# Kernel optimization log

Measured on AMD Instinct MI355X. Metric: run time of the kernel, lower is better.

## Reference

```python
import jax, jax.numpy as jnp
import numpy as np

N_POINTS, D_EMBED, N_CLUSTERS = 131072, 512, 512
ALPHA = 100.0   # softmax sharpness (python scalar in original forward)
LAMBD = 0.1     # loss weight (init arg in original)


def setup_inputs() -> dict:
    key = jax.random.key(0)
    k1, k2 = jax.random.split(key)
    embeddings = jax.random.normal(k1, (N_POINTS, D_EMBED), dtype=jnp.float32)
    centroids = jax.random.normal(k2, (N_CLUSTERS, D_EMBED), dtype=jnp.float32)
    alpha = jnp.float32(ALPHA)
    lambd = jnp.float32(LAMBD)
    return {"embeddings": embeddings, "centroids": centroids, "alpha": alpha, "lambd": lambd}


def reference(embeddings, centroids, alpha, lambd):
    # Squared euclidean distance to every centroid, computed via GEMM expansion
    # instead of the original per-centroid python loop:
    #   dist[n, k] = ||x_n||^2 - 2 x_n . c_k + ||c_k||^2
    x2 = jnp.sum(embeddings * embeddings, axis=1, keepdims=True)   # [N, 1]
    c2 = jnp.sum(centroids * centroids, axis=1)                    # [K]
    dist = x2 - 2.0 * (embeddings @ centroids.T) + c2[None, :]     # [N, K]
    # Original: exp(-alpha*(d - min_k d)) / sum == stable softmax of -alpha*d over k.
    w = jax.nn.softmax(-alpha * dist, axis=1)                      # [N, K]
    # lambd * mean over points of softmax-weighted distance sum over clusters.
    return lambd * jnp.mean(jnp.sum(dist * w, axis=1))
```

## Files before the change

kernel.cpp:

```cpp
#include <hip/hip_runtime.h>
#include <stdint.h>

#define NPTS   131072
#define DEMB   512
#define NCL    512
#define BM     64
#define NCHUNK 8
#define NTHREADS 256
#define NBLK   (NPTS / BM)

typedef __attribute__((ext_vector_type(4))) float f32x4;
typedef __attribute__((ext_vector_type(8))) short short8;
typedef __attribute__((ext_vector_type(8))) unsigned short us8;

#define WS_CB   0u
#define WS_C2   (512u * 1024u)
#define WS_PART (WS_C2 + 2048u)

static __device__ __forceinline__ unsigned short f2bf(float f) {
  union { float f; uint32_t u; } c{f};
  uint32_t r = c.u + 0x7FFFu + ((c.u >> 16) & 1u);
  return (unsigned short)(r >> 16);
}
static __device__ __forceinline__ float sq4(f32x4 v) {
  return v[0] * v[0] + v[1] * v[1] + v[2] * v[2] + v[3] * v[3];
}

#define LOAD_B8(DST, BASE)                                                     \
  do {                                                                         \
    const uint8_t* _b0 = (const uint8_t*)(BASE);                               \
    const uint8_t* _b1 = _b0 + 4096;                                           \
    asm volatile("global_load_dwordx4 %0, %8, off\n\t"                         \
                 "global_load_dwordx4 %1, %8, off offset:1024\n\t"             \
                 "global_load_dwordx4 %2, %8, off offset:2048\n\t"             \
                 "global_load_dwordx4 %3, %8, off offset:3072\n\t"             \
                 "global_load_dwordx4 %4, %9, off\n\t"                         \
                 "global_load_dwordx4 %5, %9, off offset:1024\n\t"             \
                 "global_load_dwordx4 %6, %9, off offset:2048\n\t"             \
                 "global_load_dwordx4 %7, %9, off offset:3072"                 \
                 : "=&v"(DST[0]), "=&v"(DST[1]), "=&v"(DST[2]), "=&v"(DST[3]), \
                   "=&v"(DST[4]), "=&v"(DST[5]), "=&v"(DST[6]), "=&v"(DST[7])  \
                 : "v"(_b0), "v"(_b1)                                          \
                 : "memory");                                                  \
  } while (0)

#define LOAD_E4(D, P)                                                          \
  asm volatile("global_load_dwordx4 %0, %4, off\n\t"                           \
               "global_load_dwordx4 %1, %4, off offset:16\n\t"                 \
               "global_load_dwordx4 %2, %4, off offset:32\n\t"                 \
               "global_load_dwordx4 %3, %4, off offset:48"                     \
               : "=&v"(D[0]), "=&v"(D[1]), "=&v"(D[2]), "=&v"(D[3])            \
               : "v"(P)                                                        \
               : "memory")

#define WAITV(N)                                                               \
  do {                                                                         \
    asm volatile("s_waitcnt vmcnt(" #N ")" ::: "memory");                      \
    __builtin_amdgcn_sched_barrier(0);                                         \
  } while (0)

#define BAR()                                                                  \
  do {                                                                         \
    asm volatile("s_waitcnt lgkmcnt(0)" ::: "memory");                         \
    __builtin_amdgcn_s_barrier();                                              \
  } while (0)

__global__ __launch_bounds__(128) void prep_kernel(const float* __restrict__ cent,
                                                   uint8_t* __restrict__ ws) {
  const int k = blockIdx.x;
  const int t = threadIdx.x;
  float4 v = ((const float4*)(cent + (size_t)k * DEMB))[t];
  float sq = v.x * v.x + v.y * v.y + v.z * v.z + v.w * v.w;
#pragma unroll
  for (int m = 1; m < 64; m <<= 1) sq += __shfl_xor(sq, m, 64);
  __shared__ float red[2];
  if ((t & 63) == 0) red[t >> 6] = sq;
  __syncthreads();
  if (t == 0) ((float*)(ws + WS_C2))[k] = red[0] + red[1];

  ushort4 b;
  b.x = f2bf(v.x); b.y = f2bf(v.y); b.z = f2bf(v.z); b.w = f2bf(v.w);
  const int d = t * 4;
  const int ch = d >> 6;
  const int dd = d & 63;
  const int kk = dd >> 5;
  const int lhi = (dd >> 3) & 3;
  const int elem = dd & 7;
  const int w = k >> 7;
  const int n = (k >> 4) & 7;
  const int l15 = k & 15;
  const int lane = lhi * 16 + l15;
  const uint32_t off =
      (uint32_t)((((ch * 4 + w) * 2 + kk) * 8 + n) * 64 + lane) * 16u +
      (uint32_t)elem * 2u;
  *(ushort4*)(ws + WS_CB + off) = b;
}

__global__ __launch_bounds__(NTHREADS, 2) void main_kernel(
    const float* __restrict__ emb, const uint8_t* __restrict__ ws,
    const float* __restrict__ alphap) {
  __shared__ uint8_t Ab[2][8192];
  __shared__ float redmin[256];
  __shared__ float redse[256];
  __shared__ float redsge[256];
  __shared__ float gmin[64];
  __shared__ float x2s[64];

  const int t = threadIdx.x;
  const int w = t >> 6;
  const int l = t & 63;
  const int l15 = l & 15;
  const int lhi = l >> 4;
  const int bid = blockIdx.x;
  const size_t row0 = (size_t)bid * BM;

  float* partials = (float*)(ws + WS_PART);

  f32x4 acc[4][8];
#pragma unroll
  for (int m = 0; m < 4; ++m)
#pragma unroll
    for (int n = 0; n < 8; ++n) acc[m][n] = (f32x4){0.f, 0.f, 0.f, 0.f};

  const int r = t >> 2;
  const int q = t & 3;
  const float* xge = emb + (row0 + r) * DEMB + q * 16;
  uint32_t xoff[2];
#pragma unroll
  for (int j = 0; j < 2; ++j)
    xoff[j] = (uint32_t)r * 128u + (uint32_t)(((2 * q + j) ^ (r & 7)) << 4);

  float x2a = 0.f;

  const uint8_t* fbw = ws + WS_CB + (uint32_t)w * 16384u + (uint32_t)l * 16u;

  short8 bf[16];
  f32x4 ev0[4], ev1[4];

#define STAGE_FROM(EV, DSTBUF)                                                 \
  do {                                                                         \
    uint8_t* _an = (DSTBUF);                                                   \
    _Pragma("unroll")                                                          \
    for (int j = 0; j < 2; ++j) {                                              \
      f32x4 a = EV[2 * j], b = EV[2 * j + 1];                                  \
      x2a += sq4(a) + sq4(b);                                                  \
      us8 u;                                                                   \
      u[0] = f2bf(a[0]); u[1] = f2bf(a[1]); u[2] = f2bf(a[2]); u[3] = f2bf(a[3]); \
      u[4] = f2bf(b[0]); u[5] = f2bf(b[1]); u[6] = f2bf(b[2]); u[7] = f2bf(b[3]); \
      *(us8*)(_an + xoff[j]) = u;                                              \
    }                                                                          \
  } while (0)

  LOAD_E4(ev0, xge);
  LOAD_E4(ev1, xge + 64);
  LOAD_B8((&bf[0]), fbw);
  LOAD_B8((&bf[8]), fbw + 8192);
  WAITV(20);
  STAGE_FROM(ev0, &Ab[0][0]);
  BAR();

#define CHUNK_BODY(CH, EVN, EVS, VN)                                           \
  {                                                                            \
    if ((CH) + 2 < NCHUNK)                                                     \
      LOAD_E4(EVN, xge + ((CH) + 2) * 64);                                     \
    const uint8_t* xb = &Ab[(CH) & 1][0];                                      \
    WAITV(VN);                                                                 \
    __builtin_amdgcn_s_setprio(1);                                             \
    _Pragma("unroll")                                                          \
    for (int kk = 0; kk < 2; ++kk) {                                           \
      const uint32_t swz = (uint32_t)(((kk * 4 + lhi) ^ (l15 & 7)) << 4);      \
      short8 af[4];                                                            \
      _Pragma("unroll")                                                        \
      for (int m = 0; m < 4; ++m)                                              \
        af[m] = *(const short8*)(xb + (uint32_t)(m * 16 + l15) * 128u + swz);  \
      _Pragma("unroll")                                                        \
      for (int m = 0; m < 4; ++m)                                              \
        _Pragma("unroll")                                                      \
        for (int n = 0; n < 8; ++n)                                            \
          acc[m][n] = __builtin_amdgcn_mfma_f32_16x16x32_bf16(                 \
              af[m], bf[kk * 8 + n], acc[m][n], 0, 0, 0);                      \
    }                                                                          \
    __builtin_amdgcn_s_setprio(0);                                             \
    if ((CH) + 1 < NCHUNK) {                                                   \
      STAGE_FROM(EVS, &Ab[((CH) + 1) & 1][0]);                                 \
      const uint8_t* nb = fbw + (uint32_t)((CH) + 1) * 65536u;                 \
      LOAD_B8((&bf[0]), nb);                                                   \
      LOAD_B8((&bf[8]), nb + 8192);                                            \
    }                                                                          \
    BAR();                                                                     \
  }

  CHUNK_BODY(0, ev0, ev1, 4)
  CHUNK_BODY(1, ev1, ev0, 4)
  CHUNK_BODY(2, ev0, ev1, 4)
  CHUNK_BODY(3, ev1, ev0, 4)
  CHUNK_BODY(4, ev0, ev1, 4)
  CHUNK_BODY(5, ev1, ev0, 4)
  CHUNK_BODY(6, ev0, ev1, 0)
  CHUNK_BODY(7, ev1, ev0, 0)
#undef CHUNK_BODY
#undef STAGE_FROM

  const float alpha = alphap[0];
  float c2r[8];
  {
    const float* c2p = (const float*)(ws + WS_C2) + w * 128 + l15;
    asm volatile("global_load_dword %0, %8, off\n\t"
                 "global_load_dword %1, %8, off offset:64\n\t"
                 "global_load_dword %2, %8, off offset:128\n\t"
                 "global_load_dword %3, %8, off offset:192\n\t"
                 "global_load_dword %4, %8, off offset:256\n\t"
                 "global_load_dword %5, %8, off offset:320\n\t"
                 "global_load_dword %6, %8, off offset:384\n\t"
                 "global_load_dword %7, %8, off offset:448"
                 : "=&v"(c2r[0]), "=&v"(c2r[1]), "=&v"(c2r[2]), "=&v"(c2r[3]),
                   "=&v"(c2r[4]), "=&v"(c2r[5]), "=&v"(c2r[6]), "=&v"(c2r[7])
                 : "v"(c2p)
                 : "memory");
    asm volatile("s_waitcnt vmcnt(0)" ::: "memory");
    __builtin_amdgcn_sched_barrier(0);
  }

  x2a += __shfl_xor(x2a, 1, 64);
  x2a += __shfl_xor(x2a, 2, 64);
  if ((l & 3) == 0) x2s[r] = x2a;

  float rmin[4][4];
#pragma unroll
  for (int m = 0; m < 4; ++m)
#pragma unroll
    for (int i = 0; i < 4; ++i) {
      float mn = c2r[0] - 2.f * acc[m][0][i];
#pragma unroll
      for (int n = 1; n < 8; ++n) mn = fminf(mn, c2r[n] - 2.f * acc[m][n][i]);
      rmin[m][i] = mn;
    }
#pragma unroll
  for (int msk = 1; msk < 16; msk <<= 1)
#pragma unroll
    for (int m = 0; m < 4; ++m)
#pragma unroll
      for (int i = 0; i < 4; ++i)
        rmin[m][i] = fminf(rmin[m][i], __shfl_xor(rmin[m][i], msk, 64));
  if (l15 == 0) {
#pragma unroll
    for (int m = 0; m < 4; ++m)
#pragma unroll
      for (int i = 0; i < 4; ++i)
        redmin[w * 64 + m * 16 + lhi * 4 + i] = rmin[m][i];
  }
  __syncthreads();
  if (t < 64) {
    float mn = redmin[t];
#pragma unroll
    for (int w2 = 1; w2 < 4; ++w2) mn = fminf(mn, redmin[w2 * 64 + t]);
    gmin[t] = mn;
  }
  __syncthreads();
#pragma unroll
  for (int m = 0; m < 4; ++m) {
#pragma unroll
    for (int i = 0; i < 4; ++i) {
      const int row = m * 16 + lhi * 4 + i;
      const float M = gmin[row];
      float se = 0.f, sge = 0.f;
#pragma unroll
      for (int n = 0; n < 8; ++n) {
        const float g = c2r[n] - 2.f * acc[m][n][i];
        const float gm = g - M;
        const float e = __expf(-alpha * gm);
        se += e;
        sge += gm * e;
      }
#pragma unroll
      for (int msk = 1; msk < 16; msk <<= 1) {
        se += __shfl_xor(se, msk, 64);
        sge += __shfl_xor(sge, msk, 64);
      }
      if (l15 == 0) {
        redse[w * 64 + row] = se;
        redsge[w * 64 + row] = sge;
      }
    }
  }
  __syncthreads();
  if (t < 64) {
    float Se = 0.f, Sge = 0.f;
#pragma unroll
    for (int w2 = 0; w2 < 4; ++w2) {
      Se += redse[w2 * 64 + t];
      Sge += redsge[w2 * 64 + t];
    }
    float v = gmin[t] + Sge / Se + x2s[t];
#pragma unroll
    for (int msk = 1; msk < 64; msk <<= 1) v += __shfl_xor(v, msk, 64);
    if (t == 0) partials[bid] = v;
  }
}

__global__ __launch_bounds__(256) void final_kernel(const uint8_t* __restrict__ ws,
                                                    const float* __restrict__ lambdp,
                                                    float* __restrict__ out) {
  const float* partials = (const float*)(ws + WS_PART);
  const int t = threadIdx.x;
  float s = 0.f;
  for (int i = t; i < NBLK; i += 256) s += partials[i];
#pragma unroll
  for (int msk = 1; msk < 64; msk <<= 1) s += __shfl_xor(s, msk, 64);
  __shared__ float red[4];
  if ((t & 63) == 0) red[t >> 6] = s;
  __syncthreads();
  if (t == 0)
    out[0] = lambdp[0] * (red[0] + red[1] + red[2] + red[3]) * (1.0f / (float)NPTS);
}

extern "C" void kernel_launch(void* const* d_in, const int* in_sizes, int n_in,
                              void* d_out, int out_size, void* d_ws, size_t ws_size,
                              hipStream_t stream) {
  const float* emb = (const float*)d_in[0];
  const float* cent = (const float*)d_in[1];
  const float* alphap = (const float*)d_in[2];
  const float* lambdp = (const float*)d_in[3];
  float* out = (float*)d_out;
  uint8_t* ws = (uint8_t*)d_ws;

  prep_kernel<<<NCL, 128, 0, stream>>>(cent, ws);
  main_kernel<<<NBLK, NTHREADS, 0, stream>>>(emb, ws, alphap);
  final_kernel<<<1, 256, 0, stream>>>(ws, lambdp, out);
}
```

Before: 104.0 us.

## Switch GEMM from bf16 to fp8 MFMA with double-buffered centroid fragments

```diff
diff --git a/kernel.cpp b/kernel.cpp
--- a/kernel.cpp
+++ b/kernel.cpp
@@ -10,39 +10,29 @@
 #define NBLK   (NPTS / BM)
 
 typedef __attribute__((ext_vector_type(4))) float f32x4;
-typedef __attribute__((ext_vector_type(8))) short short8;
-typedef __attribute__((ext_vector_type(8))) unsigned short us8;
 
 #define WS_CB   0u
-#define WS_C2   (512u * 1024u)
-#define WS_PART (WS_C2 + 2048u)
-
-static __device__ __forceinline__ unsigned short f2bf(float f) {
-  union { float f; uint32_t u; } c{f};
-  uint32_t r = c.u + 0x7FFFu + ((c.u >> 16) & 1u);
-  return (unsigned short)(r >> 16);
-}
+#define WS_C2   262144u
+#define WS_PART 264192u
+
 static __device__ __forceinline__ float sq4(f32x4 v) {
   return v[0] * v[0] + v[1] * v[1] + v[2] * v[2] + v[3] * v[3];
 }
 
-#define LOAD_B8(DST, BASE)                                                     \
-  do {                                                                         \
-    const uint8_t* _b0 = (const uint8_t*)(BASE);                               \
-    const uint8_t* _b1 = _b0 + 4096;                                           \
-    asm volatile("global_load_dwordx4 %0, %8, off\n\t"                         \
-                 "global_load_dwordx4 %1, %8, off offset:1024\n\t"             \
-                 "global_load_dwordx4 %2, %8, off offset:2048\n\t"             \
-                 "global_load_dwordx4 %3, %8, off offset:3072\n\t"             \
-                 "global_load_dwordx4 %4, %9, off\n\t"                         \
-                 "global_load_dwordx4 %5, %9, off offset:1024\n\t"             \
-                 "global_load_dwordx4 %6, %9, off offset:2048\n\t"             \
-                 "global_load_dwordx4 %7, %9, off offset:3072"                 \
-                 : "=&v"(DST[0]), "=&v"(DST[1]), "=&v"(DST[2]), "=&v"(DST[3]), \
-                   "=&v"(DST[4]), "=&v"(DST[5]), "=&v"(DST[6]), "=&v"(DST[7])  \
-                 : "v"(_b0), "v"(_b1)                                          \
-                 : "memory");                                                  \
-  } while (0)
+#define LOAD_B8F(DST, BASE)                                                    \
+  asm volatile("global_load_dwordx2 %0, %8, off\n\t"                           \
+               "global_load_dwordx2 %1, %8, off offset:512\n\t"                \
+               "global_load_dwordx2 %2, %8, off offset:1024\n\t"               \
+               "global_load_dwordx2 %3, %8, off offset:1536\n\t"               \
+               "global_load_dwordx2 %4, %8, off offset:2048\n\t"               \
+               "global_load_dwordx2 %5, %8, off offset:2560\n\t"               \
+               "global_load_dwordx2 %6, %8, off offset:3072\n\t"               \
+               "global_load_dwordx2 %7, %8, off offset:3584"                   \
+               : "=&v"((DST)[0]), "=&v"((DST)[1]), "=&v"((DST)[2]),            \
+                 "=&v"((DST)[3]), "=&v"((DST)[4]), "=&v"((DST)[5]),            \
+                 "=&v"((DST)[6]), "=&v"((DST)[7])                              \
+               : "v"(BASE)                                                     \
+               : "memory")
 
 #define LOAD_E4(D, P)                                                          \
   asm volatile("global_load_dwordx4 %0, %4, off\n\t"                           \
@@ -78,28 +68,27 @@
   __syncthreads();
   if (t == 0) ((float*)(ws + WS_C2))[k] = red[0] + red[1];
 
-  ushort4 b;
-  b.x = f2bf(v.x); b.y = f2bf(v.y); b.z = f2bf(v.z); b.w = f2bf(v.w);
+  int p = __builtin_amdgcn_cvt_pk_fp8_f32(v.x, v.y, 0, false);
+  p = __builtin_amdgcn_cvt_pk_fp8_f32(v.z, v.w, p, true);
+
   const int d = t * 4;
   const int ch = d >> 6;
   const int dd = d & 63;
   const int kk = dd >> 5;
   const int lhi = (dd >> 3) & 3;
-  const int elem = dd & 7;
   const int w = k >> 7;
   const int n = (k >> 4) & 7;
   const int l15 = k & 15;
   const int lane = lhi * 16 + l15;
-  const uint32_t off =
-      (uint32_t)((((ch * 4 + w) * 2 + kk) * 8 + n) * 64 + lane) * 16u +
-      (uint32_t)elem * 2u;
-  *(ushort4*)(ws + WS_CB + off) = b;
+  const uint32_t off = (uint32_t)(ch * 32768 + w * 8192 + kk * 4096 + n * 512 +
+                                  lane * 8 + (dd & 7));
+  *(uint32_t*)(ws + WS_CB + off) = (uint32_t)p;
 }
 
 __global__ __launch_bounds__(NTHREADS, 2) void main_kernel(
     const float* __restrict__ emb, const uint8_t* __restrict__ ws,
     const float* __restrict__ alphap) {
-  __shared__ uint8_t Ab[2][8192];
+  __shared__ uint8_t Ab[2][4096];
   __shared__ float redmin[256];
   __shared__ float redse[256];
   __shared__ float redsge[256];
@@ -128,13 +117,13 @@
   uint32_t xoff[2];
 #pragma unroll
   for (int j = 0; j < 2; ++j)
-    xoff[j] = (uint32_t)r * 128u + (uint32_t)(((2 * q + j) ^ (r & 7)) << 4);
+    xoff[j] = (uint32_t)r * 64u + (uint32_t)(((2 * q + j) ^ (r & 7)) << 3);
 
   float x2a = 0.f;
 
-  const uint8_t* fbw = ws + WS_CB + (uint32_t)w * 16384u + (uint32_t)l * 16u;
-
-  short8 bf[16];
+  const uint8_t* fbw = ws + WS_CB + (uint32_t)w * 8192u + (uint32_t)l * 8u;
+
+  long bA[16], bB[16];
   f32x4 ev0[4], ev1[4];
 
 #define STAGE_FROM(EV, DSTBUF)                                                 \
@@ -144,60 +133,65 @@
     for (int j = 0; j < 2; ++j) {                                              \
       f32x4 a = EV[2 * j], b = EV[2 * j + 1];                                  \
       x2a += sq4(a) + sq4(b);                                                  \
-      us8 u;                                                                   \
-      u[0] = f2bf(a[0]); u[1] = f2bf(a[1]); u[2] = f2bf(a[2]); u[3] = f2bf(a[3]); \
-      u[4] = f2bf(b[0]); u[5] = f2bf(b[1]); u[6] = f2bf(b[2]); u[7] = f2bf(b[3]); \
-      *(us8*)(_an + xoff[j]) = u;                                              \
+      uint2 u;                                                                 \
+      int p0 = __builtin_amdgcn_cvt_pk_fp8_f32(a[0], a[1], 0, false);          \
+      p0 = __builtin_amdgcn_cvt_pk_fp8_f32(a[2], a[3], p0, true);              \
+      int p1 = __builtin_amdgcn_cvt_pk_fp8_f32(b[0], b[1], 0, false);          \
+      p1 = __builtin_amdgcn_cvt_pk_fp8_f32(b[2], b[3], p1, true);              \
+      u.x = (uint32_t)p0;                                                      \
+      u.y = (uint32_t)p1;                                                      \
+      *(uint2*)(_an + xoff[j]) = u;                                            \
     }                                                                          \
   } while (0)
 
   LOAD_E4(ev0, xge);
   LOAD_E4(ev1, xge + 64);
-  LOAD_B8((&bf[0]), fbw);
-  LOAD_B8((&bf[8]), fbw + 8192);
+  LOAD_B8F(&bA[0], fbw);
+  LOAD_B8F(&bA[8], fbw + 4096);
   WAITV(20);
   STAGE_FROM(ev0, &Ab[0][0]);
   BAR();
 
-#define CHUNK_BODY(CH, EVN, EVS, VN)                                           \
+#define CHUNK_BODY(CH, BCUR, BNEXT, EVN, EVS, VN)                              \
   {                                                                            \
     if ((CH) + 2 < NCHUNK)                                                     \
       LOAD_E4(EVN, xge + ((CH) + 2) * 64);                                     \
+    if ((CH) + 1 < NCHUNK) {                                                   \
+      const uint8_t* nb = fbw + (uint32_t)((CH) + 1) * 32768u;                 \
+      LOAD_B8F(&BNEXT[0], nb);                                                 \
+      LOAD_B8F(&BNEXT[8], nb + 4096);                                          \
+    }                                                                          \
     const uint8_t* xb = &Ab[(CH) & 1][0];                                      \
     WAITV(VN);                                                                 \
     __builtin_amdgcn_s_setprio(1);                                             \
     _Pragma("unroll")                                                          \
     for (int kk = 0; kk < 2; ++kk) {                                           \
-      const uint32_t swz = (uint32_t)(((kk * 4 + lhi) ^ (l15 & 7)) << 4);      \
-      short8 af[4];                                                            \
+      const uint32_t swz = (uint32_t)(((kk * 4 + lhi) ^ (l15 & 7)) << 3);      \
+      long af[4];                                                              \
       _Pragma("unroll")                                                        \
       for (int m = 0; m < 4; ++m)                                              \
-        af[m] = *(const short8*)(xb + (uint32_t)(m * 16 + l15) * 128u + swz);  \
+        af[m] = *(const long*)(xb + (uint32_t)(m * 16 + l15) * 64u + swz);     \
       _Pragma("unroll")                                                        \
       for (int m = 0; m < 4; ++m)                                              \
         _Pragma("unroll")                                                      \
         for (int n = 0; n < 8; ++n)                                            \
-          acc[m][n] = __builtin_amdgcn_mfma_f32_16x16x32_bf16(                 \
-              af[m], bf[kk * 8 + n], acc[m][n], 0, 0, 0);                      \
+          acc[m][n] = __builtin_amdgcn_mfma_f32_16x16x32_fp8_fp8(              \
+              af[m], BCUR[kk * 8 + n], acc[m][n], 0, 0, 0);                    \
     }                                                                          \
     __builtin_amdgcn_s_setprio(0);                                             \
-    if ((CH) + 1 < NCHUNK) {                                                   \
+    if ((CH) + 1 < NCHUNK)                                                     \
       STAGE_FROM(EVS, &Ab[((CH) + 1) & 1][0]);                                 \
-      const uint8_t* nb = fbw + (uint32_t)((CH) + 1) * 65536u;                 \
-      LOAD_B8((&bf[0]), nb);                                                   \
-      LOAD_B8((&bf[8]), nb + 8192);                                            \
-    }                                                                          \
     BAR();                                                                     \
   }
 
-  CHUNK_BODY(0, ev0, ev1, 4)
-  CHUNK_BODY(1, ev1, ev0, 4)
-  CHUNK_BODY(2, ev0, ev1, 4)
-  CHUNK_BODY(3, ev1, ev0, 4)
-  CHUNK_BODY(4, ev0, ev1, 4)
-  CHUNK_BODY(5, ev1, ev0, 4)
-  CHUNK_BODY(6, ev0, ev1, 0)
-  CHUNK_BODY(7, ev1, ev0, 0)
+  CHUNK_BODY(0, bA, bB, ev0, ev1, 20)
+  CHUNK_BODY(1, bB, bA, ev1, ev0, 20)
+  CHUNK_BODY(2, bA, bB, ev0, ev1, 20)
+  CHUNK_BODY(3, bB, bA, ev1, ev0, 20)
+  CHUNK_BODY(4, bA, bB, ev0, ev1, 20)
+  CHUNK_BODY(5, bB, bA, ev1, ev0, 20)
+  CHUNK_BODY(6, bA, bB, ev0, ev1, 16)
+  CHUNK_BODY(7, bB, bA, ev1, ev0, 0)
 #undef CHUNK_BODY
 #undef STAGE_FROM
 
```

Result: faster. 99.61 us (-4.2%).
